# Optimization experiments

Measured on AMD Instinct MI355X. Metric: run time of the kernel, lower is better.

The kernel has to match this reference:

```python
import jax, jax.numpy as jnp
import numpy as np

B = 8192
N_COLS = 64
D = 1024
EPS = 1e-5


def _layernorm(x, g, b):
    m = jnp.mean(x, axis=-1, keepdims=True)
    v = jnp.mean(jnp.square(x - m), axis=-1, keepdims=True)
    return (x - m) * jax.lax.rsqrt(v + EPS) * g + b


def setup_inputs() -> dict:
    key = jax.random.key(0)
    ks = jax.random.split(key, 8)
    s = 0.02
    return {
        "x1_enc": jax.random.normal(ks[0], (1, N_COLS, D), jnp.float32),
        "x2_enc": jax.random.normal(ks[1], (B, D), jnp.float32),
        "We": jax.random.normal(ks[2], (4, 2 * D, D), jnp.float32) * s,
        "be": jnp.zeros((4, D), jnp.float32),
        "W1": jax.random.normal(ks[3], (2 * D, 4 * D), jnp.float32) * s,
        "b1": jnp.zeros((4 * D,), jnp.float32),
        "g1": jnp.ones((4 * D,), jnp.float32),
        "bt1": jnp.zeros((4 * D,), jnp.float32),
        "W2": jax.random.normal(ks[4], (4 * D, 2 * D), jnp.float32) * s,
        "b2": jnp.zeros((2 * D,), jnp.float32),
        "g2": jnp.ones((2 * D,), jnp.float32),
        "bt2": jnp.zeros((2 * D,), jnp.float32),
        "W3": jax.random.normal(ks[5], (2 * D, 1), jnp.float32) * s,
        "b3": jnp.zeros((1,), jnp.float32),
        "col_pairs": jax.random.randint(ks[6], (B, 2), 0, N_COLS, jnp.int64),
        "vis_type": jax.random.randint(ks[7], (B,), 0, 4, jnp.int64),
    }


def reference(x1_enc, x2_enc, We, be, W1, b1, g1, bt1, W2, b2, g2, bt2, W3, b3,
              col_pairs, vis_type):
    # x1 repeated B times is identical per row -> gather directly from x1_enc[0]
    x11 = x1_enc[0, col_pairs[:, 0]]          # [B, D]
    x12 = x1_enc[0, col_pairs[:, 1]]          # [B, D]
    x1c = jnp.concatenate([x11, x12], axis=1)  # [B, 2D]

    # 1-of-4 expert routing: compute all experts, select by vis_type
    all_y = jax.nn.relu(jnp.einsum('bd,edk->bek', x1c, We) + be)  # [B, 4, D]
    y1 = jnp.take_along_axis(all_y, vis_type[:, None, None], axis=1)[:, 0]  # [B, D]

    y = jnp.concatenate([y1, x2_enc], axis=1)  # [B, 2D]
    h = _layernorm(jax.nn.relu(y @ W1 + b1), g1, bt1)
    h = _layernorm(jax.nn.relu(h @ W2 + b2), g2, bt2)
    return jax.nn.sigmoid(h @ W3 + b3)  # [B, 1]
```

## Files before the change

### kernel.cpp

```cpp
#include <hip/hip_runtime.h>

typedef unsigned short u16;
typedef __bf16 bf16x8 __attribute__((ext_vector_type(8)));
typedef float f32x4v __attribute__((ext_vector_type(4)));
typedef u16 u16x8 __attribute__((ext_vector_type(8)));

__device__ __forceinline__ u16 f2bf(float f) {
  union { float f; unsigned u; } v; v.f = f;
  unsigned r = v.u + 0x7fffu + ((v.u >> 16) & 1u);
  return (u16)(r >> 16);
}
__device__ __forceinline__ float bf2f(u16 h) {
  union { unsigned u; float f; } v; v.u = ((unsigned)h) << 16;
  return v.f;
}

#define G2L16(g, l)                                                            \
  __builtin_amdgcn_global_load_lds((__attribute__((address_space(1))) void*)(g), \
                                   (__attribute__((address_space(3))) void*)(l), 16, 0, 0)

__global__ __launch_bounds__(256) void k_transpose2(const float* __restrict__ W1,
                                                    u16* __restrict__ W1T,
                                                    const float* __restrict__ W2,
                                                    u16* __restrict__ W2gT,
                                                    const float* __restrict__ g1,
                                                    const float* __restrict__ bt1,
                                                    float* __restrict__ w2ps,
                                                    float* __restrict__ w2pc) {
  __shared__ float tile[64][65];
  int bid = blockIdx.x;
  const float* in;
  u16* out;
  int R, C, bx, by, fold;
  if (bid < 2048) {
    in = W1; out = W1T; R = 2048; C = 4096; fold = 0;
    bx = bid & 63; by = bid >> 6;
  } else {
    bid -= 2048;
    in = W2; out = W2gT; R = 4096; C = 2048; fold = 1;
    bx = bid & 31; by = bid >> 5;
  }
  const int c0 = bx * 64, r0 = by * 64;
  const int t = threadIdx.x;
  const int tc = (t & 15) * 4, tr = t >> 4;
#pragma unroll
  for (int i = 0; i < 4; ++i) {
    int r = tr + i * 16;
    f32x4v v = *(const f32x4v*)(in + (size_t)(r0 + r) * C + c0 + tc);
    tile[r][tc] = v[0]; tile[r][tc + 1] = v[1];
    tile[r][tc + 2] = v[2]; tile[r][tc + 3] = v[3];
  }
  __syncthreads();
  const int oc = t >> 2;
  const int rb = (t & 3) * 16;
  float gv[16];
#pragma unroll
  for (int i = 0; i < 16; ++i) gv[i] = fold ? g1[r0 + rb + i] : 1.f;
  u16x8 o0, o1;
#pragma unroll
  for (int i = 0; i < 8; ++i) o0[i] = f2bf(tile[rb + i][oc] * gv[i]);
#pragma unroll
  for (int i = 0; i < 8; ++i) o1[i] = f2bf(tile[rb + 8 + i][oc] * gv[8 + i]);
  *(u16x8*)(out + (size_t)(c0 + oc) * R + r0 + rb) = o0;
  *(u16x8*)(out + (size_t)(c0 + oc) * R + r0 + rb + 8) = o1;
  if (fold) {
    float ps = 0.f, pc = 0.f;
#pragma unroll
    for (int i = 0; i < 16; ++i) {
      float w = tile[rb + i][oc];
      ps += gv[i] * w;
      pc += bt1[r0 + rb + i] * w;
    }
    ps += __shfl_down(ps, 2, 4); ps += __shfl_down(ps, 1, 4);
    pc += __shfl_down(pc, 2, 4); pc += __shfl_down(pc, 1, 4);
    if ((t & 3) == 0) {
      w2ps[(size_t)by * 2048 + c0 + oc] = ps;
      w2pc[(size_t)by * 2048 + c0 + oc] = pc;
    }
  }
}

__global__ __launch_bounds__(256) void k_pq(const float* __restrict__ x1,
                                            const float* __restrict__ We,
                                            float* __restrict__ pq0,
                                            float* __restrict__ pq1) {
  const int n0 = blockIdx.x * 64;
  const int ep = blockIdx.y;
  const int e = ep >> 1, p = ep & 1;
  const int khalf = blockIdx.z & 1;
  const int chalf = blockIdx.z >> 1;
  const int ks = khalf * 512;
  float* pq = khalf ? pq1 : pq0;
  __shared__ float As[32][33];
  __shared__ float Bs[32][68];
  const int t = threadIdx.x;
  const int tx = t & 15, ty = t >> 4;
  float acc[2][4] = {};
  const float* wbase = We + (size_t)e * 2048 * 1024 + (size_t)p * 1024 * 1024;
  for (int k0 = ks; k0 < ks + 512; k0 += 32) {
#pragma unroll
    for (int i = 0; i < 4; ++i) {
      int ix = t + i * 256;
      As[ix >> 5][ix & 31] =
          x1[(size_t)(chalf * 32 + (ix >> 5)) * 1024 + k0 + (ix & 31)];
    }
#pragma unroll
    for (int i = 0; i < 8; ++i) {
      int ix = t + i * 256;
      Bs[ix >> 6][ix & 63] = wbase[(size_t)(k0 + (ix >> 6)) * 1024 + n0 + (ix & 63)];
    }
    __syncthreads();
#pragma unroll
    for (int kk = 0; kk < 32; ++kk) {
      float av[2];
#pragma unroll
      for (int i = 0; i < 2; ++i) av[i] = As[ty * 2 + i][kk];
      f32x4v bv = *(const f32x4v*)&Bs[kk][tx * 4];
#pragma unroll
      for (int i = 0; i < 2; ++i)
#pragma unroll
        for (int j = 0; j < 4; ++j) acc[i][j] += av[i] * bv[j];
    }
    __syncthreads();
  }
#pragma unroll
  for (int i = 0; i < 2; ++i) {
    float* dst = pq + ((size_t)ep * 64 + chalf * 32 + ty * 2 + i) * 1024 + n0 + tx * 4;
#pragma unroll
    for (int j = 0; j < 4; ++j) dst[j] = acc[i][j];
  }
}

__global__ __launch_bounds__(256) void k_build_y(const float* __restrict__ pq0,
                                                 const float* __restrict__ pq1,
                                                 const float* __restrict__ x2,
                                                 const float* __restrict__ be,
                                                 const int* __restrict__ cp,
                                                 const int* __restrict__ vis,
                                                 u16* __restrict__ Y) {
  const int t = threadIdx.x;
  for (int rr = 0; rr < 8; ++rr) {
    const int b = blockIdx.x * 8 + rr;
    const int e = vis[b];
    u16x8 o;
    if (t < 128) {
      const int c0 = cp[2 * b], c1 = cp[2 * b + 1];
      const size_t po = ((size_t)(e * 2) * 64 + c0) * 1024 + t * 8;
      const size_t qo = ((size_t)(e * 2 + 1) * 64 + c1) * 1024 + t * 8;
      const float* B = be + e * 1024 + t * 8;
#pragma unroll
      for (int i = 0; i < 8; ++i) {
        float v = pq0[po + i] + pq1[po + i] + pq0[qo + i] + pq1[qo + i] + B[i];
        o[i] = f2bf(v > 0.f ? v : 0.f);
      }
      *(u16x8*)(Y + (size_t)b * 2048 + t * 8) = o;
    } else {
      const float* X = x2 + (size_t)b * 1024 + (size_t)(t - 128) * 8;
#pragma unroll
      for (int i = 0; i < 8; ++i) o[i] = f2bf(X[i]);
      *(u16x8*)(Y + (size_t)b * 2048 + 1024 + (size_t)(t - 128) * 8) = o;
    }
  }
}

#define BARRIER __builtin_amdgcn_s_barrier()
#define WLG0                                                    \
  do {                                                          \
    asm volatile("s_waitcnt lgkmcnt(0)" ::: "memory");          \
    __builtin_amdgcn_sched_barrier(0);                          \
  } while (0)
#define WVM(n) asm volatile("s_waitcnt vmcnt(" #n ")" ::: "memory")

template <int MODE>
__global__ __launch_bounds__(512, 2) void k_gemm(const u16* __restrict__ A,
                                                 const u16* __restrict__ BT,
                                                 const float* __restrict__ bias,
                                                 const float2* __restrict__ stats,
                                                 const float* __restrict__ s1,
                                                 const float* __restrict__ c1b,
                                                 const float* __restrict__ gw3,
                                                 float2* __restrict__ sp_out,
                                                 float4* __restrict__ part,
                                                 u16* __restrict__ C,
                                                 int M, int N, int K) {
  __shared__ u16 smem[65536];
  const int tid = threadIdx.x;
  const int lane = tid & 63;
  const int wave = tid >> 6;
  const int wm = wave >> 2;
  const int wn = wave & 3;

  const int nx = gridDim.x, ny = gridDim.y;
  const int bid = blockIdx.y * nx + blockIdx.x;
  const int stripe = ny >> 3;
  const int xcd = bid & 7;
  const int loc = bid >> 3;
  const int by = xcd * stripe + (loc % stripe);
  const int bx = loc / stripe;
  const int tileM = by * 256;
  const int tileN = bx * 256;

  f32x4v acc[8][4];
#pragma unroll
  for (int i = 0; i < 8; ++i)
#pragma unroll
    for (int j = 0; j < 4; ++j) acc[i][j] = (f32x4v){0.f, 0.f, 0.f, 0.f};

  const int srow = tid >> 3;
  const int slc = ((tid & 7) ^ (srow & 7)) * 8;
  const u16* aG = A + (size_t)(tileM + srow) * K + slc;
  const u16* bG = BT + (size_t)(tileN + srow) * K + slc;

#define STAGE(ab, h, buf, kt)                                                  \
  do {                                                                         \
    u16* dst_ = smem + (buf) * 32768 + (ab) * 16384 + (h) * 8192 + tid * 8;    \
    const u16* g_ = ((ab) ? bG : aG) + (size_t)(h) * 128 * K + (size_t)(kt) * 64; \
    G2L16(g_, dst_);                                                           \
    G2L16(g_ + (size_t)64 * K, dst_ + 4096);                                   \
  } while (0)

  const int kp0 = (((lane >> 4) ^ (lane & 7)) * 8);
  const int kp1 = kp0 ^ 32;
  const int awoff = wm * 8192 + (lane & 15) * 64;
  const int bwoff = (wn >> 1) * 8192 + ((wn & 1) * 64 + (lane & 15)) * 64;

  bf16x8 af[2][4], bf[2][4];

#define RD_A(buf, mh)                                                          \
  do {                                                                         \
    const u16* ap_ = smem + (buf) * 32768 + awoff;                             \
    _Pragma("unroll") for (int q = 0; q < 4; ++q) {                            \
      af[0][q] = *(const bf16x8*)(ap_ + ((mh) * 4 + q) * 1024 + kp0);          \
      af[1][q] = *(const bf16x8*)(ap_ + ((mh) * 4 + q) * 1024 + kp1);          \
    }                                                                          \
  } while (0)

#define RD_B(buf, nh)                                                          \
  do {                                                                         \
    const u16* bp_ = smem + (buf) * 32768 + 16384 + bwoff;                     \
    _Pragma("unroll") for (int q = 0; q < 2; ++q) {                            \
      bf[0][(nh) * 2 + q] = *(const bf16x8*)(bp_ + ((nh) * 2 + q) * 1024 + kp0); \
      bf[1][(nh) * 2 + q] = *(const bf16x8*)(bp_ + ((nh) * 2 + q) * 1024 + kp1); \
    }                                                                          \
  } while (0)

#define QUAD(mh, nh)                                                           \
  do {                                                                         \
    __builtin_amdgcn_s_setprio(1);                                             \
    _Pragma("unroll") for (int kh = 0; kh < 2; ++kh)                           \
    _Pragma("unroll") for (int q = 0; q < 4; ++q)                              \
    _Pragma("unroll") for (int p = 0; p < 2; ++p)                              \
      acc[(mh) * 4 + q][(nh) * 2 + p] = __builtin_amdgcn_mfma_f32_16x16x32_bf16( \
          af[kh][q], bf[kh][(nh) * 2 + p], acc[(mh) * 4 + q][(nh) * 2 + p], 0, 0, 0); \
    __builtin_amdgcn_s_setprio(0);                                             \
  } while (0)

  const int nkt = K >> 6;
  const int niter = nkt >> 1;

  STAGE(1, 0, 0, 0);
  STAGE(1, 1, 0, 0);
  STAGE(0, 0, 0, 0);
  STAGE(0, 1, 0, 0);
  STAGE(1, 0, 1, 1);
  STAGE(1, 1, 1, 1);
  WVM(4);
  BARRIER;

  for (int it = 0; it < niter; ++it) {
    const int t1 = 2 * it + 1;
    int t2 = 2 * it + 2; if (t2 >= nkt) t2 = nkt - 1;
    int t3 = 2 * it + 3; if (t3 >= nkt) t3 = nkt - 1;
    RD_A(0, 0); RD_B(0, 0);
    STAGE(0, 0, 1, t1);
    BARRIER; WLG0; QUAD(0, 0); BARRIER;
    RD_B(0, 1);
    STAGE(0, 1, 1, t1);
    BARRIER; WLG0; QUAD(0, 1); BARRIER;
    RD_A(0, 1);
    STAGE(1, 0, 0, t2);
    BARRIER; WLG0; QUAD(1, 0); BARRIER;
    STAGE(1, 1, 0, t2);
    BARRIER; QUAD(1, 1); WVM(4); BARRIER;
    RD_A(1, 0); RD_B(1, 0);
    STAGE(0, 0, 0, t2);
    BARRIER; WLG0; QUAD(0, 0); BARRIER;
    RD_B(1, 1);
    STAGE(0, 1, 0, t2);
    BARRIER; WLG0; QUAD(0, 1); BARRIER;
    RD_A(1, 1);
    STAGE(1, 0, 1, t3);
    BARRIER; WLG0; QUAD(1, 0); BARRIER;
    STAGE(1, 1, 1, t3);
    BARRIER; QUAD(1, 1); WVM(4); BARRIER;
  }

  const int crow = tileM + wm * 128 + (lane >> 4) * 4;
  const int ccol = tileN + wn * 64 + (lane & 15);
  float cv0[4], cv1[4], cg[4];
#pragma unroll
  for (int ni = 0; ni < 4; ++ni) {
    const int c = ccol + ni * 16;
    if (MODE == 0) {
      cv0[ni] = bias[c];
    } else {
      cv0[ni] = s1[c];
      cv1[ni] = c1b[c];
      cg[ni] = gw3[c];
    }
  }
  const int cb = bx * 4 + wn;
#pragma unroll
  for (int mi = 0; mi < 8; ++mi) {
#pragma unroll
    for (int r = 0; r < 4; ++r) {
      const int row = crow + mi * 16 + r;
      if (MODE == 0) {
        float s_ = 0.f, ss_ = 0.f;
#pragma unroll
        for (int ni = 0; ni < 4; ++ni) {
          float v = acc[mi][ni][r] + cv0[ni];
          v = v > 0.f ? v : 0.f;
          s_ += v; ss_ += v * v;
          C[(size_t)row * N + ccol + ni * 16] = f2bf(v);
        }
#pragma unroll
        for (int off = 8; off >= 1; off >>= 1) {
          s_ += __shfl_xor(s_, off, 16);
          ss_ += __shfl_xor(ss_, off, 16);
        }
        if ((lane & 15) == 0)
          sp_out[(size_t)row * 64 + cb] = make_float2(s_, ss_);
      } else {
        float2 st = stats[row];
        const float m = st.x, rs = st.y;
        float s_ = 0.f, ss_ = 0.f, d_ = 0.f;
#pragma unroll
        for (int ni = 0; ni < 4; ++ni) {
          float v = rs * acc[mi][ni][r] - rs * m * cv0[ni] + cv1[ni];
          v = v > 0.f ? v : 0.f;
          s_ += v; ss_ += v * v; d_ += v * cg[ni];
        }
#pragma unroll
        for (int off = 8; off >= 1; off >>= 1) {
          s_ += __shfl_xor(s_, off, 16);
          ss_ += __shfl_xor(ss_, off, 16);
          d_ += __shfl_xor(d_, off, 16);
        }
        if ((lane & 15) == 0)
          part[(size_t)row * 32 + cb] = make_float4(s_, ss_, d_, 0.f);
      }
    }
  }
}

__global__ __launch_bounds__(256) void k_reduce(const float2* __restrict__ sp,
                                                float2* __restrict__ stats,
                                                const float* __restrict__ w2ps,
                                                const float* __restrict__ w2pc,
                                                const float* __restrict__ b2,
                                                float* __restrict__ s1,
                                                float* __restrict__ c1b,
                                                const float* __restrict__ g2,
                                                const float* __restrict__ bt2,
                                                const float* __restrict__ W3,
                                                float* __restrict__ gw3,
                                                float* __restrict__ scal) {
  __shared__ float red[8];
  const int bid = blockIdx.x;
  const int t = threadIdx.x;
  if (bid < 32) {
    const int g = t >> 4, l = t & 15;
#pragma unroll 1
    for (int rr = 0; rr < 16; ++rr) {
      const int row = bid * 256 + rr * 16 + g;
      float s = 0.f, ss = 0.f;
#pragma unroll
      for (int i = 0; i < 4; ++i) {
        float2 p = sp[(size_t)row * 64 + l * 4 + i];
        s += p.x; ss += p.y;
      }
#pragma unroll
      for (int off = 8; off >= 1; off >>= 1) {
        s += __shfl_xor(s, off, 16);
        ss += __shfl_xor(ss, off, 16);
      }
      if (l == 0) {
        float m = s * (1.f / 4096.f);
        float var = ss * (1.f / 4096.f) - m * m;
        stats[row] = make_float2(m, rsqrtf(var + 1e-5f));
      }
    }
  } else if (bid < 40) {
    const int nn = (bid - 32) * 256 + t;
    float s = 0.f, c = 0.f;
    for (int kb = 0; kb < 64; ++kb) {
      s += w2ps[(size_t)kb * 2048 + nn];
      c += w2pc[(size_t)kb * 2048 + nn];
    }
    s1[nn] = s;
    c1b[nn] = c + b2[nn];
  } else {
    float sg = 0.f, cb = 0.f;
    for (int i = 0; i < 8; ++i) {
      int c = i * 256 + t;
      float w3 = W3[c];
      float gv = g2[c] * w3;
      gw3[c] = gv;
      sg += gv;
      cb += bt2[c] * w3;
    }
#pragma unroll
    for (int off = 32; off > 0; off >>= 1) {
      sg += __shfl_down(sg, off, 64);
      cb += __shfl_down(cb, off, 64);
    }
    const int lane = t & 63, wv = t >> 6;
    if (lane == 0) { red[wv] = sg; red[4 + wv] = cb; }
    __syncthreads();
    if (t == 0) {
      scal[0] = red[0] + red[1] + red[2] + red[3];
      scal[1] = red[4] + red[5] + red[6] + red[7];
    }
  }
}

__global__ __launch_bounds__(256) void k_final(const float4* __restrict__ part,
                                               const float* __restrict__ scal,
                                               const float* __restrict__ b3,
                                               float* __restrict__ out) {
  const int t = threadIdx.x;
  const int g = t >> 4, l = t & 15;
  const int row = blockIdx.x * 16 + g;
  float4 a = part[(size_t)row * 32 + l * 2];
  float4 b = part[(size_t)row * 32 + l * 2 + 1];
  float S = a.x + b.x, SS = a.y + b.y, D = a.z + b.z;
#pragma unroll
  for (int off = 8; off >= 1; off >>= 1) {
    S += __shfl_xor(S, off, 16);
    SS += __shfl_xor(SS, off, 16);
    D += __shfl_xor(D, off, 16);
  }
  if (l == 0) {
    float m = S * (1.f / 2048.f);
    float rs = rsqrtf(SS * (1.f / 2048.f) - m * m + 1e-5f);
    float logit = rs * D - rs * m * scal[0] + scal[1] + b3[0];
    out[row] = 1.f / (1.f + expf(-logit));
  }
}

extern "C" void kernel_launch(void* const* d_in, const int* in_sizes, int n_in,
                              void* d_out, int out_size, void* d_ws, size_t ws_size,
                              hipStream_t stream) {
  const float* x1 = (const float*)d_in[0];
  const float* x2 = (const float*)d_in[1];
  const float* We = (const float*)d_in[2];
  const float* be = (const float*)d_in[3];
  const float* W1 = (const float*)d_in[4];
  const float* b1 = (const float*)d_in[5];
  const float* g1 = (const float*)d_in[6];
  const float* bt1 = (const float*)d_in[7];
  const float* W2 = (const float*)d_in[8];
  const float* b2 = (const float*)d_in[9];
  const float* g2 = (const float*)d_in[10];
  const float* bt2 = (const float*)d_in[11];
  const float* W3 = (const float*)d_in[12];
  const float* b3 = (const float*)d_in[13];
  const int* cp = (const int*)d_in[14];
  const int* vis = (const int*)d_in[15];
  float* out = (float*)d_out;

  char* ws = (char*)d_ws;
  u16* W1T  = (u16*)(ws);
  u16* W2gT = (u16*)(ws + 16777216);
  u16* Y    = (u16*)(ws + 33554432);
  u16* H1   = (u16*)(ws + 67108864);
  float* PQ0 = (float*)(ws + 134217728);
  float* PQ1 = (float*)(ws + 136314880);
  float2* sp = (float2*)(ws + 134217728);
  float4* part = (float4*)(ws + 134217728);
  float2* stats = (float2*)(ws + 138412032);
  float* s1   = (float*)(ws + 138477568);
  float* c1b  = (float*)(ws + 138485760);
  float* w2ps = (float*)(ws + 138493952);
  float* w2pc = (float*)(ws + 139018240);
  float* gw3  = (float*)(ws + 139542528);
  float* scal = (float*)(ws + 139550720);

  k_transpose2<<<4096, 256, 0, stream>>>(W1, W1T, W2, W2gT, g1, bt1, w2ps, w2pc);
  k_pq<<<dim3(16, 8, 4), 256, 0, stream>>>(x1, We, PQ0, PQ1);
  k_build_y<<<1024, 256, 0, stream>>>(PQ0, PQ1, x2, be, cp, vis, Y);
  k_gemm<0><<<dim3(16, 32), 512, 0, stream>>>(
      Y, W1T, b1, nullptr, nullptr, nullptr, nullptr, sp, nullptr, H1,
      8192, 4096, 2048);
  k_reduce<<<41, 256, 0, stream>>>(sp, stats, w2ps, w2pc, b2, s1, c1b,
                                   g2, bt2, W3, gw3, scal);
  k_gemm<1><<<dim3(8, 32), 512, 0, stream>>>(
      H1, W2gT, nullptr, stats, s1, c1b, gw3, nullptr, part, nullptr,
      8192, 2048, 4096);
  k_final<<<512, 256, 0, stream>>>(part, scal, b3, out);
}
```

Before: 452.7 us.

## Switch GEMM to 32x32x16 bf16 MFMA with new LDS swizzle and fragment layout

Replaces the 16x16x32 MFMA tiles with 32x32x16 MFMA, so each wave holds 4x2 blocks of 16-float accumulators. The LDS swizzle, the fragment read offsets and the epilogue row/column mapping are all reworked to match, and the shuffle reductions now run across 32 lanes. It also relaxes the LDS waits with an extra lgkmcnt(8) and drops the sched_barrier. The larger MFMA is meant to cut LDS fragment reads per FLOP and raise matrix throughput. In exchange the layout math becomes more complex, with a risk of bank conflicts or wrong results.

Result: slower. 578.9 us (+27.9%).

```diff
diff --git a/kernel.cpp b/kernel.cpp
--- a/kernel.cpp
+++ b/kernel.cpp
@@ -3,6 +3,7 @@
 typedef unsigned short u16;
 typedef __bf16 bf16x8 __attribute__((ext_vector_type(8)));
 typedef float f32x4v __attribute__((ext_vector_type(4)));
+typedef float f32x16 __attribute__((ext_vector_type(16)));
 typedef u16 u16x8 __attribute__((ext_vector_type(8)));
 
 __device__ __forceinline__ u16 f2bf(float f) {
@@ -164,11 +165,8 @@
 }
 
 #define BARRIER __builtin_amdgcn_s_barrier()
-#define WLG0                                                    \
-  do {                                                          \
-    asm volatile("s_waitcnt lgkmcnt(0)" ::: "memory");          \
-    __builtin_amdgcn_sched_barrier(0);                          \
-  } while (0)
+#define WLG0 asm volatile("s_waitcnt lgkmcnt(0)" ::: "memory")
+#define WLG8 asm volatile("s_waitcnt lgkmcnt(8)" ::: "memory")
 #define WVM(n) asm volatile("s_waitcnt vmcnt(" #n ")" ::: "memory")
 
 template <int MODE>
@@ -200,14 +198,16 @@
   const int tileM = by * 256;
   const int tileN = bx * 256;
 
-  f32x4v acc[8][4];
-#pragma unroll
-  for (int i = 0; i < 8; ++i)
-#pragma unroll
-    for (int j = 0; j < 4; ++j) acc[i][j] = (f32x4v){0.f, 0.f, 0.f, 0.f};
+  f32x16 acc[4][2];
+#pragma unroll
+  for (int i = 0; i < 4; ++i)
+#pragma unroll
+    for (int j = 0; j < 2; ++j)
+#pragma unroll
+      for (int r = 0; r < 16; ++r) acc[i][j][r] = 0.f;
 
   const int srow = tid >> 3;
-  const int slc = ((tid & 7) ^ (srow & 7)) * 8;
+  const int slc = ((tid & 7) ^ ((srow ^ (srow >> 3)) & 7)) * 8;
   const u16* aG = A + (size_t)(tileM + srow) * K + slc;
   const u16* bG = BT + (size_t)(tileN + srow) * K + slc;
 
@@ -219,39 +219,46 @@
     G2L16(g_ + (size_t)64 * K, dst_ + 4096);                                   \
   } while (0)
 
-  const int kp0 = (((lane >> 4) ^ (lane & 7)) * 8);
-  const int kp1 = kp0 ^ 32;
-  const int awoff = wm * 8192 + (lane & 15) * 64;
-  const int bwoff = (wn >> 1) * 8192 + ((wn & 1) * 64 + (lane & 15)) * 64;
-
-  bf16x8 af[2][4], bf[2][4];
+  const int u_ = lane & 7;
+  const int w_ = (lane >> 3) & 3;
+  const int khi = lane >> 5;
+  int kofsE[4], kofsO[4];
+#pragma unroll
+  for (int kst = 0; kst < 4; ++kst) {
+    kofsE[kst] = ((kst * 2 + khi) ^ (u_ ^ w_)) * 8;
+    kofsO[kst] = kofsE[kst] ^ 32;
+  }
+  const int aoff = wm * 8192 + (lane & 31) * 64;
+  const int boff = 16384 + (wn >> 1) * 8192 + (wn & 1) * 4096 + (lane & 31) * 64;
+
+  bf16x8 af[2][4], bfr[2][4];
 
 #define RD_A(buf, mh)                                                          \
   do {                                                                         \
-    const u16* ap_ = smem + (buf) * 32768 + awoff;                             \
-    _Pragma("unroll") for (int q = 0; q < 4; ++q) {                            \
-      af[0][q] = *(const bf16x8*)(ap_ + ((mh) * 4 + q) * 1024 + kp0);          \
-      af[1][q] = *(const bf16x8*)(ap_ + ((mh) * 4 + q) * 1024 + kp1);          \
+    const u16* ap_ = smem + (buf) * 32768 + aoff + (mh) * 4096;                \
+    _Pragma("unroll") for (int kst = 0; kst < 4; ++kst) {                      \
+      af[0][kst] = *(const bf16x8*)(ap_ + kofsE[kst]);                         \
+      af[1][kst] = *(const bf16x8*)(ap_ + 2048 + kofsO[kst]);                  \
     }                                                                          \
   } while (0)
 
 #define RD_B(buf, nh)                                                          \
   do {                                                                         \
-    const u16* bp_ = smem + (buf) * 32768 + 16384 + bwoff;                     \
-    _Pragma("unroll") for (int q = 0; q < 2; ++q) {                            \
-      bf[0][(nh) * 2 + q] = *(const bf16x8*)(bp_ + ((nh) * 2 + q) * 1024 + kp0); \
-      bf[1][(nh) * 2 + q] = *(const bf16x8*)(bp_ + ((nh) * 2 + q) * 1024 + kp1); \
-    }                                                                          \
+    const u16* bp_ = smem + (buf) * 32768 + boff + (nh) * 2048;                \
+    _Pragma("unroll") for (int kst = 0; kst < 4; ++kst)                        \
+      bfr[nh][kst] =                                                           \
+          *(const bf16x8*)(bp_ + ((nh) ? kofsO[kst] : kofsE[kst]));            \
   } while (0)
 
 #define QUAD(mh, nh)                                                           \
   do {                                                                         \
     __builtin_amdgcn_s_setprio(1);                                             \
-    _Pragma("unroll") for (int kh = 0; kh < 2; ++kh)                           \
-    _Pragma("unroll") for (int q = 0; q < 4; ++q)                              \
-    _Pragma("unroll") for (int p = 0; p < 2; ++p)                              \
-      acc[(mh) * 4 + q][(nh) * 2 + p] = __builtin_amdgcn_mfma_f32_16x16x32_bf16( \
-          af[kh][q], bf[kh][(nh) * 2 + p], acc[(mh) * 4 + q][(nh) * 2 + p], 0, 0, 0); \
+    _Pragma("unroll") for (int kst = 0; kst < 4; ++kst) {                      \
+      acc[(mh) * 2][nh] = __builtin_amdgcn_mfma_f32_32x32x16_bf16(             \
+          af[0][kst], bfr[nh][kst], acc[(mh) * 2][nh], 0, 0, 0);               \
+      acc[(mh) * 2 + 1][nh] = __builtin_amdgcn_mfma_f32_32x32x16_bf16(         \
+          af[1][kst], bfr[nh][kst], acc[(mh) * 2 + 1][nh], 0, 0, 0);           \
+    }                                                                          \
     __builtin_amdgcn_s_setprio(0);                                             \
   } while (0)
 
@@ -273,6 +280,7 @@
     int t3 = 2 * it + 3; if (t3 >= nkt) t3 = nkt - 1;
     RD_A(0, 0); RD_B(0, 0);
     STAGE(0, 0, 1, t1);
+    WLG8;
     BARRIER; WLG0; QUAD(0, 0); BARRIER;
     RD_B(0, 1);
     STAGE(0, 1, 1, t1);
@@ -284,6 +292,7 @@
     BARRIER; QUAD(1, 1); WVM(4); BARRIER;
     RD_A(1, 0); RD_B(1, 0);
     STAGE(0, 0, 0, t2);
+    WLG8;
     BARRIER; WLG0; QUAD(0, 0); BARRIER;
     RD_B(1, 1);
     STAGE(0, 1, 0, t2);
@@ -295,59 +304,50 @@
     BARRIER; QUAD(1, 1); WVM(4); BARRIER;
   }
 
-  const int crow = tileM + wm * 128 + (lane >> 4) * 4;
-  const int ccol = tileN + wn * 64 + (lane & 15);
-  float cv0[4], cv1[4], cg[4];
-#pragma unroll
-  for (int ni = 0; ni < 4; ++ni) {
-    const int c = ccol + ni * 16;
-    if (MODE == 0) {
-      cv0[ni] = bias[c];
-    } else {
-      cv0[ni] = s1[c];
-      cv1[ni] = c1b[c];
-      cg[ni] = gw3[c];
-    }
-  }
+  const int colb = tileN + wn * 64 + (lane & 31);
+  const int half4 = (lane >> 5) * 4;
   const int cb = bx * 4 + wn;
-#pragma unroll
-  for (int mi = 0; mi < 8; ++mi) {
-#pragma unroll
-    for (int r = 0; r < 4; ++r) {
-      const int row = crow + mi * 16 + r;
+  float b0, b1, s10, s11, c10, c11, g0, g1;
+  if (MODE == 0) {
+    b0 = bias[colb]; b1 = bias[colb + 32];
+  } else {
+    s10 = s1[colb]; s11 = s1[colb + 32];
+    c10 = c1b[colb]; c11 = c1b[colb + 32];
+    g0 = gw3[colb]; g1 = gw3[colb + 32];
+  }
+#pragma unroll
+  for (int mt = 0; mt < 4; ++mt) {
+#pragma unroll
+    for (int j = 0; j < 16; ++j) {
+      const int row = tileM + wm * 128 + mt * 32 + (j & 3) + 8 * (j >> 2) + half4;
       if (MODE == 0) {
-        float s_ = 0.f, ss_ = 0.f;
-#pragma unroll
-        for (int ni = 0; ni < 4; ++ni) {
-          float v = acc[mi][ni][r] + cv0[ni];
-          v = v > 0.f ? v : 0.f;
-          s_ += v; ss_ += v * v;
-          C[(size_t)row * N + ccol + ni * 16] = f2bf(v);
+        float v0 = acc[mt][0][j] + b0; v0 = v0 > 0.f ? v0 : 0.f;
+        float v1 = acc[mt][1][j] + b1; v1 = v1 > 0.f ? v1 : 0.f;
+        C[(size_t)row * N + colb] = f2bf(v0);
+        C[(size_t)row * N + colb + 32] = f2bf(v1);
+        float s_ = v0 + v1, ss_ = v0 * v0 + v1 * v1;
+#pragma unroll
+        for (int off = 16; off >= 1; off >>= 1) {
+          s_ += __shfl_xor(s_, off, 32);
+          ss_ += __shfl_xor(ss_, off, 32);
         }
-#pragma unroll
-        for (int off = 8; off >= 1; off >>= 1) {
-          s_ += __shfl_xor(s_, off, 16);
-          ss_ += __shfl_xor(ss_, off, 16);
-        }
-        if ((lane & 15) == 0)
+        if ((lane & 31) == 0)
           sp_out[(size_t)row * 64 + cb] = make_float2(s_, ss_);
       } else {
         float2 st = stats[row];
         const float m = st.x, rs = st.y;
-        float s_ = 0.f, ss_ = 0.f, d_ = 0.f;
-#pragma unroll
-        for (int ni = 0; ni < 4; ++ni) {
-          float v = rs * acc[mi][ni][r] - rs * m * cv0[ni] + cv1[ni];
-          v = v > 0.f ? v : 0.f;
-          s_ += v; ss_ += v * v; d_ += v * cg[ni];
+        float v0 = rs * acc[mt][0][j] - rs * m * s10 + c10;
+        v0 = v0 > 0.f ? v0 : 0.f;
+        float v1 = rs * acc[mt][1][j] - rs * m * s11 + c11;
+        v1 = v1 > 0.f ? v1 : 0.f;
+        float s_ = v0 + v1, ss_ = v0 * v0 + v1 * v1, d_ = v0 * g0 + v1 * g1;
+#pragma unroll
+        for (int off = 16; off >= 1; off >>= 1) {
+          s_ += __shfl_xor(s_, off, 32);
+          ss_ += __shfl_xor(ss_, off, 32);
+          d_ += __shfl_xor(d_, off, 32);
         }
-#pragma unroll
-        for (int off = 8; off >= 1; off >>= 1) {
-          s_ += __shfl_xor(s_, off, 16);
-          ss_ += __shfl_xor(ss_, off, 16);
-          d_ += __shfl_xor(d_, off, 16);
-        }
-        if ((lane & 15) == 0)
+        if ((lane & 31) == 0)
           part[(size_t)row * 32 + cb] = make_float4(s_, ss_, d_, 0.f);
       }
     }
```

## Deepen GEMM A-tile prefetch and drop split-K in expert projection

Applied to the files above, without the earlier changes.

The main GEMM loop now issues the first A half-tile load for the next k-step one phase earlier, together with the B loads, and waits on six outstanding vector-memory ops instead of four. The aim is to give global-to-LDS loads more time in flight before they are consumed. Separately, k_pq no longer splits K into two halves with separate partial buffers. Each block accumulates the full K range, so k_build_y reads one buffer instead of summing two. This halves the k_pq grid, trading parallelism in a small kernel for less partial-buffer traffic.

Result: slower. 468.9 us (+3.6%).

```diff
diff --git a/kernel.cpp b/kernel.cpp
--- a/kernel.cpp
+++ b/kernel.cpp
@@ -82,22 +82,18 @@
 
 __global__ __launch_bounds__(256) void k_pq(const float* __restrict__ x1,
                                             const float* __restrict__ We,
-                                            float* __restrict__ pq0,
-                                            float* __restrict__ pq1) {
+                                            float* __restrict__ pq) {
   const int n0 = blockIdx.x * 64;
   const int ep = blockIdx.y;
   const int e = ep >> 1, p = ep & 1;
-  const int khalf = blockIdx.z & 1;
-  const int chalf = blockIdx.z >> 1;
-  const int ks = khalf * 512;
-  float* pq = khalf ? pq1 : pq0;
+  const int chalf = blockIdx.z;
   __shared__ float As[32][33];
   __shared__ float Bs[32][68];
   const int t = threadIdx.x;
   const int tx = t & 15, ty = t >> 4;
   float acc[2][4] = {};
   const float* wbase = We + (size_t)e * 2048 * 1024 + (size_t)p * 1024 * 1024;
-  for (int k0 = ks; k0 < ks + 512; k0 += 32) {
+  for (int k0 = 0; k0 < 1024; k0 += 32) {
 #pragma unroll
     for (int i = 0; i < 4; ++i) {
       int ix = t + i * 256;
@@ -131,8 +127,7 @@
   }
 }
 
-__global__ __launch_bounds__(256) void k_build_y(const float* __restrict__ pq0,
-                                                 const float* __restrict__ pq1,
+__global__ __launch_bounds__(256) void k_build_y(const float* __restrict__ pq,
                                                  const float* __restrict__ x2,
                                                  const float* __restrict__ be,
                                                  const int* __restrict__ cp,
@@ -150,7 +145,7 @@
       const float* B = be + e * 1024 + t * 8;
 #pragma unroll
       for (int i = 0; i < 8; ++i) {
-        float v = pq0[po + i] + pq1[po + i] + pq0[qo + i] + pq1[qo + i] + B[i];
+        float v = pq[po + i] + pq[qo + i] + B[i];
         o[i] = f2bf(v > 0.f ? v : 0.f);
       }
       *(u16x8*)(Y + (size_t)b * 2048 + t * 8) = o;
@@ -224,7 +219,7 @@
   const int awoff = wm * 8192 + (lane & 15) * 64;
   const int bwoff = (wn >> 1) * 8192 + ((wn & 1) * 64 + (lane & 15)) * 64;
 
-  bf16x8 af[2][4], bf[2][4];
+  bf16x8 af[2][4], bfr[2][4];
 
 #define RD_A(buf, mh)                                                          \
   do {                                                                         \
@@ -239,8 +234,8 @@
   do {                                                                         \
     const u16* bp_ = smem + (buf) * 32768 + 16384 + bwoff;                     \
     _Pragma("unroll") for (int q = 0; q < 2; ++q) {                            \
-      bf[0][(nh) * 2 + q] = *(const bf16x8*)(bp_ + ((nh) * 2 + q) * 1024 + kp0); \
-      bf[1][(nh) * 2 + q] = *(const bf16x8*)(bp_ + ((nh) * 2 + q) * 1024 + kp1); \
+      bfr[0][(nh) * 2 + q] = *(const bf16x8*)(bp_ + ((nh) * 2 + q) * 1024 + kp0); \
+      bfr[1][(nh) * 2 + q] = *(const bf16x8*)(bp_ + ((nh) * 2 + q) * 1024 + kp1); \
     }                                                                          \
   } while (0)
 
@@ -251,7 +246,7 @@
     _Pragma("unroll") for (int q = 0; q < 4; ++q)                              \
     _Pragma("unroll") for (int p = 0; p < 2; ++p)                              \
       acc[(mh) * 4 + q][(nh) * 2 + p] = __builtin_amdgcn_mfma_f32_16x16x32_bf16( \
-          af[kh][q], bf[kh][(nh) * 2 + p], acc[(mh) * 4 + q][(nh) * 2 + p], 0, 0, 0); \
+          af[kh][q], bfr[kh][(nh) * 2 + p], acc[(mh) * 4 + q][(nh) * 2 + p], 0, 0, 0); \
     __builtin_amdgcn_s_setprio(0);                                             \
   } while (0)
 
@@ -264,7 +259,8 @@
   STAGE(0, 1, 0, 0);
   STAGE(1, 0, 1, 1);
   STAGE(1, 1, 1, 1);
-  WVM(4);
+  STAGE(0, 0, 1, 1);
+  WVM(6);
   BARRIER;
 
   for (int it = 0; it < niter; ++it) {
@@ -272,27 +268,27 @@
     int t2 = 2 * it + 2; if (t2 >= nkt) t2 = nkt - 1;
     int t3 = 2 * it + 3; if (t3 >= nkt) t3 = nkt - 1;
     RD_A(0, 0); RD_B(0, 0);
-    STAGE(0, 0, 1, t1);
+    STAGE(0, 1, 1, t1);
     BARRIER; WLG0; QUAD(0, 0); BARRIER;
     RD_B(0, 1);
-    STAGE(0, 1, 1, t1);
     BARRIER; WLG0; QUAD(0, 1); BARRIER;
     RD_A(0, 1);
     STAGE(1, 0, 0, t2);
     BARRIER; WLG0; QUAD(1, 0); BARRIER;
     STAGE(1, 1, 0, t2);
-    BARRIER; QUAD(1, 1); WVM(4); BARRIER;
+    STAGE(0, 0, 0, t2);
+    BARRIER; QUAD(1, 1); WVM(6); BARRIER;
     RD_A(1, 0); RD_B(1, 0);
-    STAGE(0, 0, 0, t2);
+    STAGE(0, 1, 0, t2);
     BARRIER; WLG0; QUAD(0, 0); BARRIER;
     RD_B(1, 1);
-    STAGE(0, 1, 0, t2);
     BARRIER; WLG0; QUAD(0, 1); BARRIER;
     RD_A(1, 1);
     STAGE(1, 0, 1, t3);
     BARRIER; WLG0; QUAD(1, 0); BARRIER;
     STAGE(1, 1, 1, t3);
-    BARRIER; QUAD(1, 1); WVM(4); BARRIER;
+    STAGE(0, 0, 1, t3);
+    BARRIER; QUAD(1, 1); WVM(6); BARRIER;
   }
 
   const int crow = tileM + wm * 128 + (lane >> 4) * 4;
@@ -475,8 +471,7 @@
   u16* W2gT = (u16*)(ws + 16777216);
   u16* Y    = (u16*)(ws + 33554432);
   u16* H1   = (u16*)(ws + 67108864);
-  float* PQ0 = (float*)(ws + 134217728);
-  float* PQ1 = (float*)(ws + 136314880);
+  float* PQ = (float*)(ws + 134217728);
   float2* sp = (float2*)(ws + 134217728);
   float4* part = (float4*)(ws + 134217728);
   float2* stats = (float2*)(ws + 138412032);
@@ -488,8 +483,8 @@
   float* scal = (float*)(ws + 139550720);
 
   k_transpose2<<<4096, 256, 0, stream>>>(W1, W1T, W2, W2gT, g1, bt1, w2ps, w2pc);
-  k_pq<<<dim3(16, 8, 4), 256, 0, stream>>>(x1, We, PQ0, PQ1);
-  k_build_y<<<1024, 256, 0, stream>>>(PQ0, PQ1, x2, be, cp, vis, Y);
+  k_pq<<<dim3(16, 8, 2), 256, 0, stream>>>(x1, We, PQ);
+  k_build_y<<<1024, 256, 0, stream>>>(PQ, x2, be, cp, vis, Y);
   k_gemm<0><<<dim3(16, 32), 512, 0, stream>>>(
       Y, W1T, b1, nullptr, nullptr, nullptr, nullptr, sp, nullptr, H1,
       8192, 4096, 2048);
```
